# Kernel optimization log

Hardware: AMD Instinct MI355X
Metric: run time of the kernel (lower is better)

## Reference

```python
import jax, jax.numpy as jnp
import numpy as np

B, S, D, H, DFF = 2, 2048, 1024, 16, 4096
DK = D // H
EPS = 1e-6


def setup_inputs() -> dict:
    key = jax.random.key(0)
    ks = jax.random.split(key, 16)
    s = lambda fan_in: 1.0 / np.sqrt(fan_in)
    inp = {
        "xb": jax.random.normal(ks[0], (B, S, D), jnp.float32),
        "mask": jnp.ones((B, 1, 1, S), jnp.int32),
        "Wq": jax.random.normal(ks[1], (D, D), jnp.float32) * s(D),
        "bq": jnp.zeros((D,), jnp.float32),
        "Wk": jax.random.normal(ks[2], (D, D), jnp.float32) * s(D),
        "bk": jnp.zeros((D,), jnp.float32),
        "Wv": jax.random.normal(ks[3], (D, D), jnp.float32) * s(D),
        "bv": jnp.zeros((D,), jnp.float32),
        "Wo": jax.random.normal(ks[4], (D, D), jnp.float32) * s(D),
        "bo": jnp.zeros((D,), jnp.float32),
        "W1": jax.random.normal(ks[5], (D, DFF), jnp.float32) * s(D),
        "b1": jnp.zeros((DFF,), jnp.float32),
        "W2": jax.random.normal(ks[6], (DFF, D), jnp.float32) * s(DFF),
        "b2": jnp.zeros((D,), jnp.float32),
        "a1": jnp.ones((1,), jnp.float32),
        "o1": jnp.zeros((1,), jnp.float32),
        "a2": jnp.ones((1,), jnp.float32),
        "o2": jnp.zeros((1,), jnp.float32),
    }
    return inp


def layernorm(x, alpha, bias):
    # matches LayerNormalization: unbiased std (torch default), scalar alpha/bias,
    # division by (std + eps)
    mean = jnp.mean(x, axis=-1, keepdims=True)
    var = jnp.sum((x - mean) ** 2, axis=-1, keepdims=True) / (x.shape[-1] - 1)
    std = jnp.sqrt(var)
    return alpha * (x - mean) / (std + EPS) + bias


def mha(x, mask, Wq, bq, Wk, bk, Wv, bv, Wo, bo):
    b, s, d = x.shape
    q = (x @ Wq + bq).reshape(b, s, H, DK).transpose(0, 2, 1, 3)  # [B,H,S,DK]
    k = (x @ Wk + bk).reshape(b, s, H, DK).transpose(0, 2, 1, 3)
    v = (x @ Wv + bv).reshape(b, s, H, DK).transpose(0, 2, 1, 3)
    logits = jnp.einsum("bhqd,bhkd->bhqk", q, k) / np.sqrt(DK)
    logits = jnp.where(mask == 0, jnp.float32(-1e9), logits)
    probs = jax.nn.softmax(logits, axis=-1)
    a = jnp.einsum("bhqk,bhkd->bhqd", probs, v)  # [B,H,S,DK]
    a = a.transpose(0, 2, 1, 3).reshape(b, s, d)
    return a @ Wo + bo


def reference(xb, mask, Wq, bq, Wk, bk, Wv, bv, Wo, bo, W1, b1, W2, b2, a1, o1, a2, o2):
    # residual 1: x + MHA(LN(x))  (dropout disabled: eval mode)
    h = xb + mha(layernorm(xb, a1, o1), mask, Wq, bq, Wk, bk, Wv, bv, Wo, bo)
    # residual 2: h + FFN(LN(h))
    z = layernorm(h, a2, o2)
    ff = jax.nn.relu(z @ W1 + b1) @ W2 + b2
    return h + ff
```

## Files before the change

### kernel.cpp

```cpp
#include <hip/hip_runtime.h>
#include <hip/hip_bf16.h>
#include <math.h>

typedef __bf16 bf16x8 __attribute__((ext_vector_type(8)));
typedef float f32x4 __attribute__((ext_vector_type(4)));
typedef float f32x16 __attribute__((ext_vector_type(16)));
typedef unsigned short u16;

#define DEV __device__ __forceinline__

static constexpr int Bc = 2, Sc = 2048, Dc = 1024, Hc = 16, DFFc = 4096, DKc = 64;
static constexpr int Mc = Bc * Sc;
static constexpr float QSCALE = 0.125f * 1.4426950408889634f;

DEV u16 f32_to_bf16(float x) {
    unsigned u = __builtin_bit_cast(unsigned, x);
    u += 0x7FFFu + ((u >> 16) & 1u);
    return (u16)(u >> 16);
}

DEV float bf16_to_f32(u16 h) {
    return __builtin_bit_cast(float, (unsigned)h << 16);
}

DEV float exp2_fast(float x) {
    float r;
    asm("v_exp_f32 %0, %1" : "=v"(r) : "v"(x));
    return r;
}

DEV unsigned cvt_pk_bf16(float lo, float hi_) {
    unsigned r;
    asm("v_cvt_pk_bf16_f32 %0, %1, %2" : "=v"(r) : "v"(lo), "v"(hi_));
    return r;
}

DEV void gload_lds16(const u16* g, u16* l) {
    __builtin_amdgcn_global_load_lds(
        (const __attribute__((address_space(1))) void*)g,
        (__attribute__((address_space(3))) void*)l, 16, 0, 0);
}

DEV float block_reduce_sum(float v) {
    __shared__ float part[4];
    int lane = threadIdx.x & 63, w = threadIdx.x >> 6;
    #pragma unroll
    for (int m = 1; m < 64; m <<= 1) v += __shfl_xor(v, m);
    __syncthreads();
    if (lane == 0) part[w] = v;
    __syncthreads();
    return part[0] + part[1] + part[2] + part[3];
}

__global__ __launch_bounds__(256)
void ln_kernel(const float* __restrict__ x, u16* __restrict__ y,
               const float* __restrict__ alpha, const float* __restrict__ beta) {
    long row = blockIdx.x;
    const float4 v = reinterpret_cast<const float4*>(x + row * Dc)[threadIdx.x];
    float s = v.x + v.y + v.z + v.w;
    s = block_reduce_sum(s);
    float mean = s * (1.0f / Dc);
    float d0 = v.x - mean, d1 = v.y - mean, d2 = v.z - mean, d3 = v.w - mean;
    float ss = d0*d0 + d1*d1 + d2*d2 + d3*d3;
    ss = block_reduce_sum(ss);
    float stdv = sqrtf(ss / (float)(Dc - 1));
    float sc = alpha[0] / (stdv + 1e-6f);
    float bi = beta[0];
    ushort4 o;
    o.x = f32_to_bf16(d0 * sc + bi);
    o.y = f32_to_bf16(d1 * sc + bi);
    o.z = f32_to_bf16(d2 * sc + bi);
    o.w = f32_to_bf16(d3 * sc + bi);
    reinterpret_cast<ushort4*>(y + row * Dc)[threadIdx.x] = o;
}

__global__ void transpose_conv_kernel(const float* __restrict__ in, u16* __restrict__ out,
                                      int K, int N) {
    __shared__ float tile[32][33];
    int k0 = blockIdx.y * 32, n0 = blockIdx.x * 32;
    int tx = threadIdx.x, ty = threadIdx.y;
    #pragma unroll
    for (int i = 0; i < 4; i++)
        tile[ty + i*8][tx] = in[(long)(k0 + ty + i*8) * N + n0 + tx];
    __syncthreads();
    #pragma unroll
    for (int i = 0; i < 4; i++)
        out[(long)(n0 + ty + i*8) * K + k0 + tx] = f32_to_bf16(tile[tx][ty + i*8]);
}

__global__ __launch_bounds__(256)
void mbias_kernel(const int* __restrict__ mask, float* __restrict__ mbias) {
    int i = blockIdx.x * 256 + threadIdx.x;
    mbias[i] = mask[i] ? 0.f : -1e9f;
}

enum { EPI_QKV = 0, EPI_RELU = 1, EPI_RES = 2 };

template<int EPI, int BM, int BN, bool DB>
__global__ __launch_bounds__(256, 3)
void gemm_kernel(const u16* __restrict__ A, const u16* __restrict__ BT,
                 const float* __restrict__ b0, const float* __restrict__ b1,
                 const float* __restrict__ b2, void* __restrict__ outp,
                 const float* __restrict__ res, int M, int N, int K) {
    constexpr int BK = 64, RI = BM / 32, RJ = BN / 32;
    constexpr int NB = DB ? 2 : 1;
    __shared__ u16 As[NB][BM * BK];
    __shared__ u16 Bs[NB][BN * BK];
    const int tid = threadIdx.x;
    const int wave = tid >> 6, lane = tid & 63;
    const int wr = wave >> 1, wc = wave & 1;
    const int lr = lane & 15, lg = lane >> 4;
    const int m0 = blockIdx.y * BM, n0 = blockIdx.x * BN;
    const int z = blockIdx.z;
    const u16* Bz = BT + (size_t)z * N * K;
    const int srow = lane >> 3, scol = (lane & 7) * 8;

    f32x4 acc[RI][RJ] = {};

    const u16* ap[RI];
    const u16* bp[RJ];
    #pragma unroll
    for (int i = 0; i < RI; i++) ap[i] = A  + (size_t)(m0 + (wave*RI + i)*8 + srow) * K + scol;
    #pragma unroll
    for (int j = 0; j < RJ; j++) bp[j] = Bz + (size_t)(n0 + (wave*RJ + j)*8 + srow) * K + scol;

    auto stage = [&](int bi, int kt) {
        #pragma unroll
        for (int i = 0; i < RI; i++) gload_lds16(ap[i] + kt, &As[bi][(wave*RI + i) * 512]);
        #pragma unroll
        for (int j = 0; j < RJ; j++) gload_lds16(bp[j] + kt, &Bs[bi][(wave*RJ + j) * 512]);
    };
    auto compute = [&](int bi) {
        #pragma unroll
        for (int ks = 0; ks < BK; ks += 32) {
            bf16x8 a[RI], b[RJ];
            #pragma unroll
            for (int i = 0; i < RI; i++)
                a[i] = *reinterpret_cast<const bf16x8*>(&As[bi][(wr*(BM/2) + i*16 + lr) * BK + ks + lg*8]);
            #pragma unroll
            for (int j = 0; j < RJ; j++)
                b[j] = *reinterpret_cast<const bf16x8*>(&Bs[bi][(wc*(BN/2) + j*16 + lr) * BK + ks + lg*8]);
            #pragma unroll
            for (int i = 0; i < RI; i++)
                #pragma unroll
                for (int j = 0; j < RJ; j++)
                    acc[i][j] = __builtin_amdgcn_mfma_f32_16x16x32_bf16(a[i], b[j], acc[i][j], 0, 0, 0);
        }
    };

    if constexpr (DB) {
        const int nT = K / BK;
        stage(0, 0);
        __syncthreads();
        for (int t = 0; t < nT; t++) {
            const int cur = t & 1;
            if (t + 1 < nT) stage(cur ^ 1, (t + 1) * BK);
            compute(cur);
            __syncthreads();
        }
    } else {
        for (int kt = 0; kt < K; kt += BK) {
            stage(0, kt);
            __syncthreads();
            compute(0);
            __syncthreads();
        }
    }

    const float* bias = (EPI == EPI_QKV) ? (z == 0 ? b0 : z == 1 ? b1 : b2) : b0;
    #pragma unroll
    for (int i = 0; i < RI; i++) {
        #pragma unroll
        for (int j = 0; j < RJ; j++) {
            const int col = n0 + wc*(BN/2) + j*16 + lr;
            const float bv = bias[col];
            #pragma unroll
            for (int rg = 0; rg < 4; rg++) {
                const int row = m0 + wr*(BM/2) + i*16 + lg*4 + rg;
                float val = acc[i][j][rg] + bv;
                if constexpr (EPI == EPI_QKV) {
                    int bb = row >> 11, s = row & (Sc - 1);
                    int hh = col >> 6, dk = col & 63;
                    u16* o = (u16*)outp + (size_t)z * Mc * Dc;
                    if (z == 2)
                        o[((size_t)(bb * Hc + hh) * DKc + dk) * Sc + s] = f32_to_bf16(val);
                    else
                        o[(((size_t)(bb * Hc + hh) * Sc + s) << 6) + dk] =
                            f32_to_bf16(z == 0 ? val * QSCALE : val);
                } else if constexpr (EPI == EPI_RELU) {
                    ((u16*)outp)[(size_t)row * N + col] = f32_to_bf16(fmaxf(val, 0.0f));
                } else {
                    size_t idx = (size_t)row * N + col;
                    ((float*)outp)[idx] = res[idx] + val;
                }
            }
        }
    }
}

__global__ __launch_bounds__(256, 4)
void attn_kernel(const u16* __restrict__ Qg, const u16* __restrict__ Kg,
                 const u16* __restrict__ VTg, const float* __restrict__ mbias,
                 u16* __restrict__ part, float2* __restrict__ ml) {
    constexpr int KVB = 64, NT = (Sc / 2) / KVB;
    __shared__ u16 Ks[2][KVB * DKc];
    __shared__ u16 VTs[2][KVB * DKc];
    __shared__ float mbs[Sc / 2];

    const int tid = threadIdx.x;
    const int wave = tid >> 6, lane = tid & 63;
    const int l31 = lane & 31, hi = lane >> 5;
    const int bh = blockIdx.y, b = bh >> 4, hh = bh & 15;
    const int q0 = blockIdx.x * 128 + wave * 32;
    const int z = blockIdx.z, kv0 = z * (Sc / 2);
    const long base = (long)bh * Sc * DKc;

    *reinterpret_cast<float4*>(&mbs[tid * 4]) =
        *reinterpret_cast<const float4*>(&mbias[b * Sc + kv0 + tid * 4]);

    bf16x8 qf[4];
    {
        const u16* qrow = Qg + base + (long)(q0 + l31) * DKc + hi * 8;
        #pragma unroll
        for (int s = 0; s < 4; s++)
            qf[s] = *reinterpret_cast<const bf16x8*>(qrow + s * 16);
    }

    const int unit0 = wave * 128 + lane;
    const int r0 = unit0 >> 3, u0 = unit0 & 7;
    const int c8 = (u0 ^ (r0 & 7)) * 8;
    const u16* ksrc = Kg  + base + (size_t)(kv0 + r0) * DKc + c8;
    const u16* vsrc = VTg + base + (size_t)r0 * Sc + kv0 + c8;

    auto stage = [&](int bi, int kt) {
        gload_lds16(ksrc + (size_t)kt * DKc,       &Ks [bi][wave * 1024]);
        gload_lds16(ksrc + (size_t)(kt + 8) * DKc, &Ks [bi][wave * 1024 + 512]);
        gload_lds16(vsrc + kt,                     &VTs[bi][wave * 1024]);
        gload_lds16(vsrc + kt + 8 * Sc,            &VTs[bi][wave * 1024 + 512]);
    };

    stage(0, 0);
    __syncthreads();

    f32x16 accO[2] = {};
    float mrun = -3.0e38f, lrun = 0.f;

    for (int t = 0; t < NT; t++) {
        const int cur = t & 1;
        if (t + 1 < NT) stage(cur ^ 1, (t + 1) * KVB);

        f32x16 st[2];
        #pragma unroll
        for (int kt2 = 0; kt2 < 2; kt2++) {
            f32x16 s = {};
            const int row = kt2 * 32 + l31;
            #pragma unroll
            for (int step = 0; step < 4; step++) {
                const int unit = (step * 2 + hi) ^ (row & 7);
                bf16x8 kf = *reinterpret_cast<const bf16x8*>(&Ks[cur][row * DKc + unit * 8]);
                s = __builtin_amdgcn_mfma_f32_32x32x16_bf16(kf, qf[step], s, 0, 0, 0);
            }
            st[kt2] = s;
        }

        float pm = -3.0e38f;
        #pragma unroll
        for (int kt2 = 0; kt2 < 2; kt2++) {
            #pragma unroll
            for (int g = 0; g < 4; g++) {
                const float4 mb = *reinterpret_cast<const float4*>(
                    &mbs[t * KVB + kt2 * 32 + g * 8 + hi * 4]);
                st[kt2][g*4+0] += mb.x;
                st[kt2][g*4+1] += mb.y;
                st[kt2][g*4+2] += mb.z;
                st[kt2][g*4+3] += mb.w;
                pm = fmaxf(fmaxf(pm, st[kt2][g*4+0]), st[kt2][g*4+1]);
                pm = fmaxf(fmaxf(pm, st[kt2][g*4+2]), st[kt2][g*4+3]);
            }
        }
        pm = fmaxf(pm, __shfl_xor(pm, 32));

        if (__any(pm - mrun > 11.54f)) {
            const float mnew = fmaxf(mrun, pm);
            const float corr = exp2_fast(mrun - mnew);
            mrun = mnew; lrun *= corr;
            #pragma unroll
            for (int r = 0; r < 16; r++) {
                accO[0][r] *= corr;
                accO[1][r] *= corr;
            }
        }

        float rsum = 0.f;
        #pragma unroll
        for (int kt2 = 0; kt2 < 2; kt2++)
            #pragma unroll
            for (int r = 0; r < 16; r++) {
                const float p = exp2_fast(st[kt2][r] - mrun);
                st[kt2][r] = p;
                rsum += p;
            }
        rsum += __shfl_xor(rsum, 32);
        lrun += rsum;

        #pragma unroll
        for (int kt2 = 0; kt2 < 2; kt2++) {
            #pragma unroll
            for (int kstep = 0; kstep < 2; kstep++) {
                unsigned w0 = cvt_pk_bf16(st[kt2][kstep*8+0], st[kt2][kstep*8+1]);
                unsigned w1 = cvt_pk_bf16(st[kt2][kstep*8+2], st[kt2][kstep*8+3]);
                unsigned w2 = cvt_pk_bf16(st[kt2][kstep*8+4], st[kt2][kstep*8+5]);
                unsigned w3 = cvt_pk_bf16(st[kt2][kstep*8+6], st[kt2][kstep*8+7]);
                const unsigned p0 = (unsigned)__shfl_xor((int)w0, 32);
                const unsigned p1 = (unsigned)__shfl_xor((int)w1, 32);
                const unsigned p2 = (unsigned)__shfl_xor((int)w2, 32);
                const unsigned p3 = (unsigned)__shfl_xor((int)w3, 32);
                uint4 e;
                e.x = hi ? p2 : w0;
                e.y = hi ? p3 : w1;
                e.z = hi ? w2 : p0;
                e.w = hi ? w3 : p1;
                const bf16x8 pa = __builtin_bit_cast(bf16x8, e);
                #pragma unroll
                for (int dt = 0; dt < 2; dt++) {
                    const int drow = dt * 32 + l31;
                    const int unit = (kt2 * 4 + kstep * 2 + hi) ^ (drow & 7);
                    bf16x8 vf = *reinterpret_cast<const bf16x8*>(&VTs[cur][drow * DKc + unit * 8]);
                    accO[dt] = __builtin_amdgcn_mfma_f32_32x32x16_bf16(pa, vf, accO[dt], 0, 0, 0);
                }
            }
        }
        __syncthreads();
    }

    u16* pz = part + (size_t)z * Mc * Dc;
    #pragma unroll
    for (int r = 0; r < 16; r++) {
        const int qr = (r & 3) + 8 * (r >> 2) + 4 * hi;
        u16* po = pz + ((long)(b * Sc + q0 + qr)) * Dc + hh * 64;
        po[l31]      = f32_to_bf16(accO[0][r]);
        po[32 + l31] = f32_to_bf16(accO[1][r]);
    }
    if (hi == 0)
        ml[((size_t)z * Bc * Hc + bh) * Sc + q0 + l31] = float2{mrun, lrun};
}

__global__ __launch_bounds__(256)
void combine_kernel(const u16* __restrict__ part, const float2* __restrict__ ml,
                    u16* __restrict__ Aout) {
    const int idx = blockIdx.x * 256 + threadIdx.x;
    const int row = idx >> 7, g = idx & 127, d0 = g * 8;
    const int b = row >> 11, s = row & (Sc - 1), hh = d0 >> 6;
    const int bh = b * Hc + hh;
    const float2 ab0 = ml[(size_t)bh * Sc + s];
    const float2 ab1 = ml[((size_t)Bc * Hc + bh) * Sc + s];
    const float m = fmaxf(ab0.x, ab1.x);
    const float w0 = exp2_fast(ab0.x - m), w1 = exp2_fast(ab1.x - m);
    const float rinv = 1.0f / (w0 * ab0.y + w1 * ab1.y);
    const uint4 pa = *reinterpret_cast<const uint4*>(part + (size_t)row * Dc + d0);
    const uint4 pb = *reinterpret_cast<const uint4*>(part + (size_t)Mc * Dc + (size_t)row * Dc + d0);
    const u16* ha = (const u16*)&pa;
    const u16* hb = (const u16*)&pb;
    ushort4 o[2];
    #pragma unroll
    for (int h = 0; h < 2; h++) {
        #pragma unroll
        for (int e = 0; e < 4; e++) {
            float v = (w0 * bf16_to_f32(ha[h*4+e]) + w1 * bf16_to_f32(hb[h*4+e])) * rinv;
            (&o[h].x)[e] = f32_to_bf16(v);
        }
    }
    *reinterpret_cast<ushort4*>(Aout + (size_t)row * Dc + d0)     = o[0];
    *reinterpret_cast<ushort4*>(Aout + (size_t)row * Dc + d0 + 4) = o[1];
}

extern "C" void kernel_launch(void* const* d_in, const int* in_sizes, int n_in,
                              void* d_out, int out_size, void* d_ws, size_t ws_size,
                              hipStream_t stream) {
    (void)in_sizes; (void)n_in; (void)out_size; (void)ws_size;
    const float* xb = (const float*)d_in[0];
    const int*  mask = (const int*)d_in[1];
    const float* Wq = (const float*)d_in[2];
    const float* bq = (const float*)d_in[3];
    const float* Wk = (const float*)d_in[4];
    const float* bk = (const float*)d_in[5];
    const float* Wv = (const float*)d_in[6];
    const float* bv = (const float*)d_in[7];
    const float* Wo = (const float*)d_in[8];
    const float* bo = (const float*)d_in[9];
    const float* W1 = (const float*)d_in[10];
    const float* b1 = (const float*)d_in[11];
    const float* W2 = (const float*)d_in[12];
    const float* b2 = (const float*)d_in[13];
    const float* a1 = (const float*)d_in[14];
    const float* o1 = (const float*)d_in[15];
    const float* a2 = (const float*)d_in[16];
    const float* o2 = (const float*)d_in[17];
    float* out = (float*)d_out;

    char* p = (char*)d_ws;
    auto alloc = [&](size_t bytes) { char* r = p; p += (bytes + 255) & ~(size_t)255; return r; };
    u16* xln   = (u16*)alloc((size_t)Mc * Dc * 2);
    u16* WTqkv = (u16*)alloc((size_t)3 * Dc * Dc * 2);
    u16* WTo   = (u16*)alloc((size_t)Dc * Dc * 2);
    u16* WT1   = (u16*)alloc((size_t)Dc * DFFc * 2);
    u16* WT2   = (u16*)alloc((size_t)DFFc * Dc * 2);
    u16* qkv   = (u16*)alloc((size_t)3 * Mc * Dc * 2);
    u16* Aat   = (u16*)alloc((size_t)Mc * Dc * 2);
    float* hbuf = (float*)alloc((size_t)Mc * Dc * 4);
    u16* zb  = (u16*)alloc((size_t)Mc * Dc * 2);
    u16* ffh = (u16*)alloc((size_t)Mc * DFFc * 2);

    u16*    apart = (u16*)ffh;
    float2* aml   = (float2*)hbuf;
    float*  mbias = (float*)((char*)hbuf + (size_t)2 * 1024 * 1024);

    dim3 blkT(32, 8);
    transpose_conv_kernel<<<dim3(Dc/32,   Dc/32),   blkT, 0, stream>>>(Wq, WTqkv,             Dc, Dc);
    transpose_conv_kernel<<<dim3(Dc/32,   Dc/32),   blkT, 0, stream>>>(Wk, WTqkv + Dc*Dc,     Dc, Dc);
    transpose_conv_kernel<<<dim3(Dc/32,   Dc/32),   blkT, 0, stream>>>(Wv, WTqkv + 2*Dc*Dc,   Dc, Dc);
    transpose_conv_kernel<<<dim3(Dc/32,   Dc/32),   blkT, 0, stream>>>(Wo, WTo, Dc, Dc);
    transpose_conv_kernel<<<dim3(DFFc/32, Dc/32),   blkT, 0, stream>>>(W1, WT1, Dc, DFFc);
    transpose_conv_kernel<<<dim3(Dc/32,   DFFc/32), blkT, 0, stream>>>(W2, WT2, DFFc, Dc);

    mbias_kernel<<<(Bc * Sc) / 256, 256, 0, stream>>>(mask, mbias);
    ln_kernel<<<Mc, 256, 0, stream>>>(xb, xln, a1, o1);

    gemm_kernel<EPI_QKV, 128, 128, false><<<dim3(Dc/128, Mc/128, 3), 256, 0, stream>>>(
        xln, WTqkv, bq, bk, bv, qkv, nullptr, Mc, Dc, Dc);

    attn_kernel<<<dim3(Sc/128, Bc*Hc, 2), 256, 0, stream>>>(
        qkv, qkv + (size_t)Mc*Dc, qkv + (size_t)2*Mc*Dc, mbias, apart, aml);

    combine_kernel<<<(Mc * Dc / 8) / 256, 256, 0, stream>>>(apart, aml, Aat);

    gemm_kernel<EPI_RES, 128, 64, true><<<dim3(Dc/64, Mc/128), 256, 0, stream>>>(
        Aat, WTo, bo, nullptr, nullptr, hbuf, xb, Mc, Dc, Dc);

    ln_kernel<<<Mc, 256, 0, stream>>>(hbuf, zb, a2, o2);

    gemm_kernel<EPI_RELU, 128, 128, false><<<dim3(DFFc/128, Mc/128), 256, 0, stream>>>(
        zb, WT1, b1, nullptr, nullptr, ffh, nullptr, Mc, DFFc, Dc);

    gemm_kernel<EPI_RES, 128, 64, true><<<dim3(Dc/64, Mc/128), 256, 0, stream>>>(
        ffh, WT2, b2, nullptr, nullptr, out, hbuf, Mc, Dc, DFFc);
}
```

Measured before the change: 279.9 us.

## Merge weight transposes into one launch, fold mask bias, swizzle GEMM LDS

Replaces the six per-weight transpose launches with a single kernel covering all weights through a linear block index, and drops the separate mask-bias kernel by converting the int mask to a float bias inside the attention kernel. It also XOR-swizzles the GEMM shared-memory column layout on both the staging and fragment-read side to reduce LDS bank conflicts. Together these cut launch count and LDS conflicts. The combined transpose assumes the weights sit contiguously in the workspace, since WTo, WT1 and WT2 are now written as offsets from WTqkv.

```diff
diff --git a/kernel.cpp b/kernel.cpp
--- a/kernel.cpp
+++ b/kernel.cpp
@@ -74,24 +74,34 @@
     reinterpret_cast<ushort4*>(y + row * Dc)[threadIdx.x] = o;
 }
 
-__global__ void transpose_conv_kernel(const float* __restrict__ in, u16* __restrict__ out,
-                                      int K, int N) {
+__global__ void transpose_all_kernel(const float* __restrict__ Wq, const float* __restrict__ Wk,
+                                     const float* __restrict__ Wv, const float* __restrict__ Wo,
+                                     const float* __restrict__ W1, const float* __restrict__ W2,
+                                     u16* __restrict__ out) {
     __shared__ float tile[32][33];
-    int k0 = blockIdx.y * 32, n0 = blockIdx.x * 32;
-    int tx = threadIdx.x, ty = threadIdx.y;
+    const int id = blockIdx.x;
+    const float* in; u16* o; int N, t;
+    if (id < 4096) {
+        const int w = id >> 10; t = id & 1023;
+        in = w == 0 ? Wq : w == 1 ? Wk : w == 2 ? Wv : Wo;
+        o = out + (size_t)w * 1024 * 1024;
+        N = 1024;
+    } else if (id < 8192) {
+        t = id - 4096; in = W1; o = out + (size_t)4 * 1024 * 1024; N = 4096;
+    } else {
+        t = id - 8192; in = W2; o = out + (size_t)8 * 1024 * 1024; N = 1024;
+    }
+    const int ntx = N >> 5;
+    const int n0 = (t % ntx) * 32, k0 = (t / ntx) * 32;
+    const int K = (id >= 8192) ? 4096 : 1024;
+    const int tx = threadIdx.x, ty = threadIdx.y;
     #pragma unroll
     for (int i = 0; i < 4; i++)
         tile[ty + i*8][tx] = in[(long)(k0 + ty + i*8) * N + n0 + tx];
     __syncthreads();
     #pragma unroll
     for (int i = 0; i < 4; i++)
-        out[(long)(n0 + ty + i*8) * K + k0 + tx] = f32_to_bf16(tile[tx][ty + i*8]);
-}
-
-__global__ __launch_bounds__(256)
-void mbias_kernel(const int* __restrict__ mask, float* __restrict__ mbias) {
-    int i = blockIdx.x * 256 + threadIdx.x;
-    mbias[i] = mask[i] ? 0.f : -1e9f;
+        o[(long)(n0 + ty + i*8) * K + k0 + tx] = f32_to_bf16(tile[tx][ty + i*8]);
 }
 
 enum { EPI_QKV = 0, EPI_RELU = 1, EPI_RES = 2 };
@@ -112,8 +122,10 @@
     const int lr = lane & 15, lg = lane >> 4;
     const int m0 = blockIdx.y * BM, n0 = blockIdx.x * BN;
     const int z = blockIdx.z;
-    const u16* Bz = BT + (size_t)z * N * K;
-    const int srow = lane >> 3, scol = (lane & 7) * 8;
+    const u16* Bz = (EPI == EPI_QKV) ? BT + (size_t)z * N * K : BT;
+
+    const int srow = lane >> 3;
+    const int scol = ((lane & 7) ^ srow) * 8;
 
     f32x4 acc[RI][RJ] = {};
 
@@ -133,13 +145,14 @@
     auto compute = [&](int bi) {
         #pragma unroll
         for (int ks = 0; ks < BK; ks += 32) {
+            const int u = (((ks >> 3) + lg) ^ (lr & 7)) * 8;
             bf16x8 a[RI], b[RJ];
             #pragma unroll
             for (int i = 0; i < RI; i++)
-                a[i] = *reinterpret_cast<const bf16x8*>(&As[bi][(wr*(BM/2) + i*16 + lr) * BK + ks + lg*8]);
+                a[i] = *reinterpret_cast<const bf16x8*>(&As[bi][(wr*(BM/2) + i*16 + lr) * BK + u]);
             #pragma unroll
             for (int j = 0; j < RJ; j++)
-                b[j] = *reinterpret_cast<const bf16x8*>(&Bs[bi][(wc*(BN/2) + j*16 + lr) * BK + ks + lg*8]);
+                b[j] = *reinterpret_cast<const bf16x8*>(&Bs[bi][(wc*(BN/2) + j*16 + lr) * BK + u]);
             #pragma unroll
             for (int i = 0; i < RI; i++)
                 #pragma unroll
@@ -200,7 +213,7 @@
 
 __global__ __launch_bounds__(256, 4)
 void attn_kernel(const u16* __restrict__ Qg, const u16* __restrict__ Kg,
-                 const u16* __restrict__ VTg, const float* __restrict__ mbias,
+                 const u16* __restrict__ VTg, const int* __restrict__ mask,
                  u16* __restrict__ part, float2* __restrict__ ml) {
     constexpr int KVB = 64, NT = (Sc / 2) / KVB;
     __shared__ u16 Ks[2][KVB * DKc];
@@ -215,8 +228,15 @@
     const int z = blockIdx.z, kv0 = z * (Sc / 2);
     const long base = (long)bh * Sc * DKc;
 
-    *reinterpret_cast<float4*>(&mbs[tid * 4]) =
-        *reinterpret_cast<const float4*>(&mbias[b * Sc + kv0 + tid * 4]);
+    {
+        const int4 mv = *reinterpret_cast<const int4*>(&mask[b * Sc + kv0 + tid * 4]);
+        float4 f;
+        f.x = mv.x ? 0.f : -1e9f;
+        f.y = mv.y ? 0.f : -1e9f;
+        f.z = mv.z ? 0.f : -1e9f;
+        f.w = mv.w ? 0.f : -1e9f;
+        *reinterpret_cast<float4*>(&mbs[tid * 4]) = f;
+    }
 
     bf16x8 qf[4];
     {
@@ -410,27 +430,20 @@
     float* hbuf = (float*)alloc((size_t)Mc * Dc * 4);
     u16* zb  = (u16*)alloc((size_t)Mc * Dc * 2);
     u16* ffh = (u16*)alloc((size_t)Mc * DFFc * 2);
+    (void)WTo; (void)WT1;
 
     u16*    apart = (u16*)ffh;
     float2* aml   = (float2*)hbuf;
-    float*  mbias = (float*)((char*)hbuf + (size_t)2 * 1024 * 1024);
-
-    dim3 blkT(32, 8);
-    transpose_conv_kernel<<<dim3(Dc/32,   Dc/32),   blkT, 0, stream>>>(Wq, WTqkv,             Dc, Dc);
-    transpose_conv_kernel<<<dim3(Dc/32,   Dc/32),   blkT, 0, stream>>>(Wk, WTqkv + Dc*Dc,     Dc, Dc);
-    transpose_conv_kernel<<<dim3(Dc/32,   Dc/32),   blkT, 0, stream>>>(Wv, WTqkv + 2*Dc*Dc,   Dc, Dc);
-    transpose_conv_kernel<<<dim3(Dc/32,   Dc/32),   blkT, 0, stream>>>(Wo, WTo, Dc, Dc);
-    transpose_conv_kernel<<<dim3(DFFc/32, Dc/32),   blkT, 0, stream>>>(W1, WT1, Dc, DFFc);
-    transpose_conv_kernel<<<dim3(Dc/32,   DFFc/32), blkT, 0, stream>>>(W2, WT2, DFFc, Dc);
-
-    mbias_kernel<<<(Bc * Sc) / 256, 256, 0, stream>>>(mask, mbias);
+
+    transpose_all_kernel<<<12288, dim3(32, 8), 0, stream>>>(Wq, Wk, Wv, Wo, W1, W2, WTqkv);
+
     ln_kernel<<<Mc, 256, 0, stream>>>(xb, xln, a1, o1);
 
     gemm_kernel<EPI_QKV, 128, 128, false><<<dim3(Dc/128, Mc/128, 3), 256, 0, stream>>>(
         xln, WTqkv, bq, bk, bv, qkv, nullptr, Mc, Dc, Dc);
 
     attn_kernel<<<dim3(Sc/128, Bc*Hc, 2), 256, 0, stream>>>(
-        qkv, qkv + (size_t)Mc*Dc, qkv + (size_t)2*Mc*Dc, mbias, apart, aml);
+        qkv, qkv + (size_t)Mc*Dc, qkv + (size_t)2*Mc*Dc, mask, apart, aml);
 
     combine_kernel<<<(Mc * Dc / 8) / 256, 256, 0, stream>>>(apart, aml, Aat);
 
```

After: 240.1 us. 1.17x faster.
